# Performance work log

Hardware: AMD Instinct MI355X
Metric: run time of the kernel (lower is better)

## Reference

```python
import jax, jax.numpy as jnp
import numpy as np

N = 100_000
E = 1_600_000
D = 128
LN_EPS = 1e-5


def _gcn_layer(x, src, dst, W, b, gamma, beta):
    # GCNConv (PyG defaults): linear transform, add self-loops, symmetric norm,
    # scatter-add aggregation, then bias. Followed by LayerNorm + ReLU.
    n = x.shape[0]
    h = x @ W  # [N, out]
    loop = jnp.arange(n, dtype=src.dtype)
    src_f = jnp.concatenate([src, loop])  # [E+N]
    dst_f = jnp.concatenate([dst, loop])
    deg = jax.ops.segment_sum(jnp.ones(src_f.shape[0], dtype=h.dtype), dst_f, num_segments=n)
    dinv = jnp.where(deg > 0, jax.lax.rsqrt(deg), 0.0)
    norm = dinv[src_f] * dinv[dst_f]  # [E+N]
    msg = h[src_f] * norm[:, None]  # [E+N, out] -- dominant HBM traffic
    out = jax.ops.segment_sum(msg, dst_f, num_segments=n) + b
    # LayerNorm over feature dim
    mu = jnp.mean(out, axis=-1, keepdims=True)
    var = jnp.mean(jnp.square(out - mu), axis=-1, keepdims=True)
    ln = (out - mu) * jax.lax.rsqrt(var + LN_EPS) * gamma + beta
    # ReLU; dropout is identity in eval mode
    return jax.nn.relu(ln)


def setup_inputs() -> dict:
    key = jax.random.key(0)
    ks = jax.random.split(key, 10)
    x = jax.random.normal(ks[0], (N, D), dtype=jnp.float32)
    edge_index = jax.random.randint(ks[1], (2, E), 0, N, dtype=jnp.int32)
    s = 1.0 / np.sqrt(D)
    W1 = jax.random.normal(ks[2], (D, D), dtype=jnp.float32) * s
    b1 = jnp.zeros((D,), dtype=jnp.float32)
    g1 = jnp.ones((D,), dtype=jnp.float32)
    be1 = jnp.zeros((D,), dtype=jnp.float32)
    W2 = jax.random.normal(ks[3], (D, D), dtype=jnp.float32) * s
    b2 = jnp.zeros((D,), dtype=jnp.float32)
    g2 = jnp.ones((D,), dtype=jnp.float32)
    be2 = jnp.zeros((D,), dtype=jnp.float32)
    return {"x": x, "edge_index": edge_index, "W1": W1, "b1": b1, "g1": g1,
            "be1": be1, "W2": W2, "b2": b2, "g2": g2, "be2": be2}


def reference(x, edge_index, W1, b1, g1, be1, W2, b2, g2, be2):
    src, dst = edge_index[0], edge_index[1]  # PyG flow: source_to_target
    h = _gcn_layer(x, src, dst, W1, b1, g1, be1)
    h = _gcn_layer(h, src, dst, W2, b2, g2, be2)
    return h
```

## Files before the change

### kernel.cpp

```cpp
#include <hip/hip_runtime.h>

#define D 128
#define NBSHIFT 10
#define NB (1 << NBSHIFT)
#define EPB 2048

typedef __attribute__((ext_vector_type(8))) short bf16x8;
typedef __attribute__((ext_vector_type(4))) float floatx4;

__device__ __forceinline__ float bflo(unsigned int u){ return __uint_as_float(u << 16); }
__device__ __forceinline__ float bfhi(unsigned int u){ return __uint_as_float(u & 0xffff0000u); }
__device__ __forceinline__ unsigned int f2bfbits(float f){
    unsigned int x = __float_as_uint(f);
    return (x + 0x7fffu + ((x >> 16) & 1u)) >> 16;
}

__global__ __launch_bounds__(256) void k_bcount(const int* __restrict__ dst, int* __restrict__ bcnt, int E){
    __shared__ int hist[128];
    int t = threadIdx.x;
    int base = blockIdx.x * EPB;
    if (t < 128) hist[t] = 0;
    __syncthreads();
#pragma unroll
    for (int j = 0; j < 8; ++j){
        int e = base + j * 256 + t;
        if (e < E) atomicAdd(&hist[dst[e] >> NBSHIFT], 1);
    }
    __syncthreads();
    if (t < 128 && hist[t] > 0) atomicAdd(&bcnt[t], hist[t]);
}

__global__ void k_bscan(const int* __restrict__ bcnt, int* __restrict__ bbase, int* __restrict__ bcur,
                        int* __restrict__ rowStartN, int NBK){
    if (threadIdx.x == 0){
        int run = 0;
        for (int b = 0; b < NBK; ++b){ bbase[b] = run; bcur[b] = run; run += bcnt[b]; }
        bbase[NBK] = run;
        *rowStartN = run;
    }
}

__global__ __launch_bounds__(256) void k_bucket(const int* __restrict__ src, const int* __restrict__ dst,
                                                int* __restrict__ bcur, unsigned int* __restrict__ edge1,
                                                int NBK, int E){
    __shared__ int hist[128], lstart[128], lcur[128], gbase[128];
    __shared__ unsigned int stage[EPB];
    int t = threadIdx.x;
    int base = blockIdx.x * EPB;
    int tot = min(EPB, E - base);
    if (t < 128) hist[t] = 0;
    __syncthreads();

    unsigned int ent[8]; int bk[8]; int cnt = 0;
#pragma unroll
    for (int j = 0; j < 8; ++j){
        int e = base + j * 256 + t;
        if (e < base + tot){
            unsigned s = (unsigned)src[e], d = (unsigned)dst[e];
            ent[cnt] = s | ((d & (NB - 1)) << 20);
            bk[cnt] = (int)(d >> NBSHIFT);
            atomicAdd(&hist[bk[cnt]], 1);
            ++cnt;
        }
    }
    __syncthreads();
    if (t < 128) lstart[t] = hist[t];
    __syncthreads();
    for (int off = 1; off < 128; off <<= 1){
        int v = 0;
        if (t < 128 && t >= off) v = lstart[t - off];
        __syncthreads();
        if (t < 128) lstart[t] += v;
        __syncthreads();
    }
    if (t < 128){
        int ex = lstart[t] - hist[t];
        lstart[t] = ex;
        lcur[t] = ex;
        if (t < NBK && hist[t] > 0) gbase[t] = atomicAdd(&bcur[t], hist[t]);
    }
    __syncthreads();
    for (int j = 0; j < cnt; ++j){
        int pos = atomicAdd(&lcur[bk[j]], 1);
        stage[pos] = ent[j];
    }
    __syncthreads();
    for (int i = t; i < tot; i += 256){
        unsigned int e1 = stage[i];
        int b = (int)((e1 >> 20) & (NB - 1));
        int lo = 0, hi = 127;
        while (lo < hi){
            int midb = (lo + hi + 1) >> 1;
            if (lstart[midb] <= i) lo = midb; else hi = midb - 1;
        }
        b = lo;
        edge1[gbase[b] + (i - lstart[b])] = e1;
    }
}

__global__ __launch_bounds__(1024) void k_csr2(const unsigned int* __restrict__ edge1,
                                               const int* __restrict__ bbase,
                                               int* __restrict__ rowStart, float* __restrict__ dinv,
                                               int* __restrict__ csr, int N){
    __shared__ int hist[NB];
    __shared__ int sc[NB];
    int b = blockIdx.x, t = threadIdx.x;
    int nbase = b << NBSHIFT;
    int nn = min(N - nbase, NB);
    int ebeg = bbase[b], eend = bbase[b + 1];

    if (t < NB) hist[t] = 0;
    __syncthreads();
    for (int i = ebeg + t; i < eend; i += 1024)
        atomicAdd(&hist[edge1[i] >> 20], 1);
    __syncthreads();
    if (t < NB) sc[t] = hist[t];
    __syncthreads();
    for (int off = 1; off < NB; off <<= 1){
        int v = (t >= off && t < NB) ? sc[t - off] : 0;
        __syncthreads();
        if (t < NB) sc[t] += v;
        __syncthreads();
    }
    if (t < NB){
        int cur = ebeg + sc[t] - hist[t];
        sc[t] = cur;
        if (t < nn){
            rowStart[nbase + t] = cur;
            dinv[nbase + t] = rsqrtf((float)hist[t] + 1.0f);
        }
    }
    __syncthreads();
    for (int i = ebeg + t; i < eend; i += 1024){
        unsigned int p = edge1[i];
        int pos = atomicAdd(&sc[p >> 20], 1);
        csr[pos] = (int)(p & 0xFFFFFu);
    }
}

__global__ __launch_bounds__(256) void k_wtrans(const float* __restrict__ W1,
                                                const float* __restrict__ W2,
                                                unsigned short* __restrict__ Wt1,
                                                unsigned short* __restrict__ Wt2){
    int i = blockIdx.x * 256 + threadIdx.x;
    const float* Ws; unsigned short* Wd; int j = i;
    if (i < 16384){ Ws = W1; Wd = Wt1; } else { Ws = W2; Wd = Wt2; j -= 16384; }
    int k = j >> 7, n = j & 127;
    Wd[n * 128 + k] = (unsigned short)f2bfbits(Ws[k * 128 + n]);
}

template<bool A_BF16>
__global__ __launch_bounds__(256) void k_gemm(const void* __restrict__ Av,
                                              const unsigned short* __restrict__ Wt,
                                              unsigned short* __restrict__ Hout, int Nrows){
    int wave = threadIdx.x >> 6, lane = threadIdx.x & 63;
    int m = lane & 15, quad = lane >> 4;
    int row0 = blockIdx.x * 64 + wave * 16;
    int arow = row0 + m;
    int arowc = arow < Nrows ? arow : Nrows - 1;

    bf16x8 a[4];
    if (A_BF16){
        const unsigned short* Ap = (const unsigned short*)Av + (size_t)arowc * D + quad * 8;
#pragma unroll
        for (int kt = 0; kt < 4; ++kt) a[kt] = *(const bf16x8*)(Ap + kt * 32);
    } else {
        const float* Ap = (const float*)Av + (size_t)arowc * D + quad * 8;
#pragma unroll
        for (int kt = 0; kt < 4; ++kt){
            float4 v0 = *(const float4*)(Ap + kt * 32);
            float4 v1 = *(const float4*)(Ap + kt * 32 + 4);
            bf16x8 af;
            af[0] = (short)f2bfbits(v0.x); af[1] = (short)f2bfbits(v0.y);
            af[2] = (short)f2bfbits(v0.z); af[3] = (short)f2bfbits(v0.w);
            af[4] = (short)f2bfbits(v1.x); af[5] = (short)f2bfbits(v1.y);
            af[6] = (short)f2bfbits(v1.z); af[7] = (short)f2bfbits(v1.w);
            a[kt] = af;
        }
    }

    floatx4 acc[8];
#pragma unroll
    for (int nt = 0; nt < 8; ++nt) acc[nt] = (floatx4){0.f, 0.f, 0.f, 0.f};

    const unsigned short* Bp = Wt + m * D + quad * 8;
#pragma unroll
    for (int kt = 0; kt < 4; ++kt){
        bf16x8 bk[8];
#pragma unroll
        for (int nt = 0; nt < 8; ++nt) bk[nt] = *(const bf16x8*)(Bp + nt * 16 * D + kt * 32);
#pragma unroll
        for (int nt = 0; nt < 8; ++nt)
            acc[nt] = __builtin_amdgcn_mfma_f32_16x16x32_bf16(a[kt], bk[nt], acc[nt], 0, 0, 0);
    }
#pragma unroll
    for (int nt = 0; nt < 8; ++nt){
#pragma unroll
        for (int r = 0; r < 4; ++r){
            int rr = row0 + quad * 4 + r;
            if (rr < Nrows) Hout[(size_t)rr * D + nt * 16 + m] = (unsigned short)f2bfbits(acc[nt][r]);
        }
    }
}

template<bool OUT_BF16>
__global__ __launch_bounds__(256) void k_agg(const unsigned short* __restrict__ h,
                                             const int* __restrict__ rowStart,
                                             const int* __restrict__ csr,
                                             const float* __restrict__ dinv,
                                             const float* __restrict__ bias,
                                             const float* __restrict__ gamma,
                                             const float* __restrict__ beta,
                                             void* __restrict__ outv, int N){
    int node = blockIdx.x * 4 + (threadIdx.x >> 6);
    if (node >= N) return;
    int lane = threadIdx.x & 63;
    int half = lane >> 5, li = lane & 31;
    const uint2* hv = (const uint2*)h;

    float dv = dinv[node];
    float4 acc = {0.f, 0.f, 0.f, 0.f};
    if (half == 0){
        uint2 hs = hv[(size_t)node * 32 + li];
        float w0 = dv * dv;
        acc.x = bflo(hs.x) * w0; acc.y = bfhi(hs.x) * w0;
        acc.z = bflo(hs.y) * w0; acc.w = bfhi(hs.y) * w0;
    }

    int start = rowStart[node], end = rowStart[node + 1];
    int mid = start + ((end - start + 1) >> 1);
    int i    = half ? mid : start;
    int iend = half ? end : mid;

    for (; i + 4 <= iend; i += 4){
        int s0 = csr[i], s1 = csr[i + 1], s2 = csr[i + 2], s3 = csr[i + 3];
        uint2 h0 = hv[(size_t)s0 * 32 + li];
        uint2 h1 = hv[(size_t)s1 * 32 + li];
        uint2 h2 = hv[(size_t)s2 * 32 + li];
        uint2 h3 = hv[(size_t)s3 * 32 + li];
        float w0 = dinv[s0] * dv, w1 = dinv[s1] * dv, w2 = dinv[s2] * dv, w3 = dinv[s3] * dv;
        acc.x = fmaf(bflo(h0.x), w0, acc.x); acc.y = fmaf(bfhi(h0.x), w0, acc.y);
        acc.z = fmaf(bflo(h0.y), w0, acc.z); acc.w = fmaf(bfhi(h0.y), w0, acc.w);
        acc.x = fmaf(bflo(h1.x), w1, acc.x); acc.y = fmaf(bfhi(h1.x), w1, acc.y);
        acc.z = fmaf(bflo(h1.y), w1, acc.z); acc.w = fmaf(bfhi(h1.y), w1, acc.w);
        acc.x = fmaf(bflo(h2.x), w2, acc.x); acc.y = fmaf(bfhi(h2.x), w2, acc.y);
        acc.z = fmaf(bflo(h2.y), w2, acc.z); acc.w = fmaf(bfhi(h2.y), w2, acc.w);
        acc.x = fmaf(bflo(h3.x), w3, acc.x); acc.y = fmaf(bfhi(h3.x), w3, acc.y);
        acc.z = fmaf(bflo(h3.y), w3, acc.z); acc.w = fmaf(bfhi(h3.y), w3, acc.w);
    }
    for (; i < iend; ++i){
        int s = csr[i];
        float ws = dinv[s] * dv;
        uint2 hs = hv[(size_t)s * 32 + li];
        acc.x = fmaf(bflo(hs.x), ws, acc.x); acc.y = fmaf(bfhi(hs.x), ws, acc.y);
        acc.z = fmaf(bflo(hs.y), ws, acc.z); acc.w = fmaf(bfhi(hs.y), ws, acc.w);
    }

    acc.x += __shfl_xor(acc.x, 32, 64);
    acc.y += __shfl_xor(acc.y, 32, 64);
    acc.z += __shfl_xor(acc.z, 32, 64);
    acc.w += __shfl_xor(acc.w, 32, 64);

    float4 bb = ((const float4*)bias)[li];
    acc.x += bb.x; acc.y += bb.y; acc.z += bb.z; acc.w += bb.w;

    float s1 = acc.x + acc.y + acc.z + acc.w;
    float s2 = acc.x * acc.x + acc.y * acc.y + acc.z * acc.z + acc.w * acc.w;
#pragma unroll
    for (int off = 16; off > 0; off >>= 1){
        s1 += __shfl_xor(s1, off, 64);
        s2 += __shfl_xor(s2, off, 64);
    }
    float mu = s1 * (1.0f / 128.0f);
    float var = s2 * (1.0f / 128.0f) - mu * mu;
    float rstd = rsqrtf(var + 1e-5f);

    float4 gg = ((const float4*)gamma)[li];
    float4 be = ((const float4*)beta)[li];
    float ox = fmaxf(fmaf((acc.x - mu) * rstd, gg.x, be.x), 0.0f);
    float oy = fmaxf(fmaf((acc.y - mu) * rstd, gg.y, be.y), 0.0f);
    float oz = fmaxf(fmaf((acc.z - mu) * rstd, gg.z, be.z), 0.0f);
    float ow = fmaxf(fmaf((acc.w - mu) * rstd, gg.w, be.w), 0.0f);
    if (half == 0){
        if (OUT_BF16){
            uint2 o;
            o.x = f2bfbits(ox) | (f2bfbits(oy) << 16);
            o.y = f2bfbits(oz) | (f2bfbits(ow) << 16);
            ((uint2*)outv)[(size_t)node * 32 + li] = o;
        } else {
            floatx4 o = {ox, oy, oz, ow};
            __builtin_nontemporal_store(o, (floatx4*)outv + (size_t)node * 32 + li);
        }
    }
}

extern "C" void kernel_launch(void* const* d_in, const int* in_sizes, int n_in,
                              void* d_out, int out_size, void* d_ws, size_t ws_size,
                              hipStream_t stream){
    const float* x   = (const float*)d_in[0];
    const int*   ei  = (const int*)d_in[1];
    const float* W1  = (const float*)d_in[2];
    const float* b1  = (const float*)d_in[3];
    const float* g1  = (const float*)d_in[4];
    const float* be1 = (const float*)d_in[5];
    const float* W2  = (const float*)d_in[6];
    const float* b2  = (const float*)d_in[7];
    const float* g2  = (const float*)d_in[8];
    const float* be2 = (const float*)d_in[9];
    float* out = (float*)d_out;

    const int N = in_sizes[0] / D;
    const int E = in_sizes[1] / 2;
    const int* src = ei;
    const int* dst = ei + E;

    char* w = (char*)d_ws;
    size_t off = 0;
    auto alloc = [&](size_t bytes) -> char* {
        char* p = w + off;
        off = (off + bytes + 255) & ~(size_t)255;
        return p;
    };
    const int NBK = (N + NB - 1) >> NBSHIFT;
    int*            bcnt     = (int*)alloc((size_t)NBK * 4);
    int*            bbase    = (int*)alloc((size_t)(NBK + 1) * 4);
    int*            bcur     = (int*)alloc((size_t)NBK * 4);
    int*            rowStart = (int*)alloc((size_t)(N + 1) * 4);
    float*          dinv     = (float*)alloc((size_t)N * 4);
    unsigned int*   edge1    = (unsigned int*)alloc((size_t)E * 4);
    int*            csr      = (int*)alloc((size_t)E * 4);
    unsigned short* wt1      = (unsigned short*)alloc(16384 * 2);
    unsigned short* wt2      = (unsigned short*)alloc(16384 * 2);
    unsigned short* h        = (unsigned short*)alloc((size_t)N * D * 2);
    unsigned short* hmid     = (unsigned short*)d_out;

    (void)hipMemsetAsync(bcnt, 0, (size_t)NBK * 4, stream);

    int gB = (E + EPB - 1) / EPB;
    int gG = (N + 63) / 64;
    int gA = (N + 3) / 4;

    k_bcount<<<gB, 256, 0, stream>>>(dst, bcnt, E);
    k_bscan <<<1, 64, 0, stream>>>(bcnt, bbase, bcur, rowStart + N, NBK);
    k_bucket<<<gB, 256, 0, stream>>>(src, dst, bcur, edge1, NBK, E);
    k_csr2  <<<NBK, 1024, 0, stream>>>(edge1, bbase, rowStart, dinv, csr, N);
    k_wtrans<<<128, 256, 0, stream>>>(W1, W2, wt1, wt2);

    k_gemm<false><<<gG, 256, 0, stream>>>(x, wt1, h, N);
    k_agg<true>  <<<gA, 256, 0, stream>>>(h, rowStart, csr, dinv, b1, g1, be1, hmid, N);
    k_gemm<true> <<<gG, 256, 0, stream>>>(hmid, wt2, h, N);
    k_agg<false> <<<gA, 256, 0, stream>>>(h, rowStart, csr, dinv, b2, g2, be2, out, N);
}
```

Measured before the change: 412.5 us.

## Use per-block histograms for deterministic bucketing and coalesce GEMM output via LDS

The edge bucketing pass drops the global atomic counter and the memset. Each block now writes its own histogram, a column-scan kernel computes per-block global offsets, and the bucket kernel writes to those precomputed positions without recounting. The GEMM swaps its operand roles so each lane holds contiguous output columns, stages results in a swizzled LDS tile, and stores full 16-byte rows coalesced instead of scattered 2-byte writes. This adds an extra hist/gloc buffer and a serial column scan over roughly 780 block rows in a single small kernel.

After: 427.0 us. 1.04x slower.

```diff
diff --git a/kernel.cpp b/kernel.cpp
--- a/kernel.cpp
+++ b/kernel.cpp
@@ -15,86 +15,99 @@
     return (x + 0x7fffu + ((x >> 16) & 1u)) >> 16;
 }
 
-__global__ __launch_bounds__(256) void k_bcount(const int* __restrict__ dst, int* __restrict__ bcnt, int E){
-    __shared__ int hist[128];
+__global__ __launch_bounds__(256) void k_bcount(const int* __restrict__ dst,
+                                                int* __restrict__ hist, int E){
+    __shared__ int h[128];
     int t = threadIdx.x;
     int base = blockIdx.x * EPB;
-    if (t < 128) hist[t] = 0;
+    if (t < 128) h[t] = 0;
     __syncthreads();
 #pragma unroll
     for (int j = 0; j < 8; ++j){
         int e = base + j * 256 + t;
-        if (e < E) atomicAdd(&hist[dst[e] >> NBSHIFT], 1);
-    }
-    __syncthreads();
-    if (t < 128 && hist[t] > 0) atomicAdd(&bcnt[t], hist[t]);
-}
-
-__global__ void k_bscan(const int* __restrict__ bcnt, int* __restrict__ bbase, int* __restrict__ bcur,
-                        int* __restrict__ rowStartN, int NBK){
-    if (threadIdx.x == 0){
-        int run = 0;
-        for (int b = 0; b < NBK; ++b){ bbase[b] = run; bcur[b] = run; run += bcnt[b]; }
-        bbase[NBK] = run;
-        *rowStartN = run;
-    }
+        if (e < E) atomicAdd(&h[dst[e] >> NBSHIFT], 1);
+    }
+    __syncthreads();
+    if (t < 128) hist[blockIdx.x * 128 + t] = h[t];
+}
+
+__global__ __launch_bounds__(128) void k_colscan(const int* __restrict__ hist, int nH,
+                                                 int* __restrict__ gloc, int* __restrict__ bbase,
+                                                 int* __restrict__ rowStartN){
+    int b = threadIdx.x;
+    int run = 0;
+    int blk = 0;
+    for (; blk + 4 <= nH; blk += 4){
+        int v0 = hist[(blk + 0) * 128 + b];
+        int v1 = hist[(blk + 1) * 128 + b];
+        int v2 = hist[(blk + 2) * 128 + b];
+        int v3 = hist[(blk + 3) * 128 + b];
+        gloc[(blk + 0) * 128 + b] = run;
+        gloc[(blk + 1) * 128 + b] = run + v0;
+        gloc[(blk + 2) * 128 + b] = run + v0 + v1;
+        gloc[(blk + 3) * 128 + b] = run + v0 + v1 + v2;
+        run += v0 + v1 + v2 + v3;
+    }
+    for (; blk < nH; ++blk){
+        int v = hist[blk * 128 + b];
+        gloc[blk * 128 + b] = run;
+        run += v;
+    }
+    __shared__ int sm[128];
+    sm[b] = run; __syncthreads();
+    for (int off = 1; off < 128; off <<= 1){
+        int x = (b >= off) ? sm[b - off] : 0;
+        __syncthreads();
+        sm[b] += x;
+        __syncthreads();
+    }
+    bbase[b] = (b > 0) ? sm[b - 1] : 0;
+    if (b == 127){ bbase[128] = sm[127]; *rowStartN = sm[127]; }
 }
 
 __global__ __launch_bounds__(256) void k_bucket(const int* __restrict__ src, const int* __restrict__ dst,
-                                                int* __restrict__ bcur, unsigned int* __restrict__ edge1,
-                                                int NBK, int E){
-    __shared__ int hist[128], lstart[128], lcur[128], gbase[128];
+                                                const int* __restrict__ hist, const int* __restrict__ gloc,
+                                                const int* __restrict__ bbase,
+                                                unsigned int* __restrict__ edge1, int E){
+    __shared__ int sc[128], lstart[128], lcur[128], gb[128];
     __shared__ unsigned int stage[EPB];
-    int t = threadIdx.x;
-    int base = blockIdx.x * EPB;
+    int t = threadIdx.x, blk = blockIdx.x;
+    int base = blk * EPB;
     int tot = min(EPB, E - base);
-    if (t < 128) hist[t] = 0;
-    __syncthreads();
-
-    unsigned int ent[8]; int bk[8]; int cnt = 0;
+    int hv = 0;
+    if (t < 128){ hv = hist[blk * 128 + t]; sc[t] = hv; }
+    __syncthreads();
+    for (int off = 1; off < 128; off <<= 1){
+        int v = (t < 128 && t >= off) ? sc[t - off] : 0;
+        __syncthreads();
+        if (t < 128) sc[t] += v;
+        __syncthreads();
+    }
+    if (t < 128){
+        int ex = sc[t] - hv;
+        lstart[t] = ex; lcur[t] = ex;
+        gb[t] = bbase[t] + gloc[blk * 128 + t];
+    }
+    __syncthreads();
 #pragma unroll
     for (int j = 0; j < 8; ++j){
         int e = base + j * 256 + t;
-        if (e < base + tot){
+        if (e < E){
             unsigned s = (unsigned)src[e], d = (unsigned)dst[e];
-            ent[cnt] = s | ((d & (NB - 1)) << 20);
-            bk[cnt] = (int)(d >> NBSHIFT);
-            atomicAdd(&hist[bk[cnt]], 1);
-            ++cnt;
-        }
-    }
-    __syncthreads();
-    if (t < 128) lstart[t] = hist[t];
-    __syncthreads();
-    for (int off = 1; off < 128; off <<= 1){
-        int v = 0;
-        if (t < 128 && t >= off) v = lstart[t - off];
-        __syncthreads();
-        if (t < 128) lstart[t] += v;
-        __syncthreads();
-    }
-    if (t < 128){
-        int ex = lstart[t] - hist[t];
-        lstart[t] = ex;
-        lcur[t] = ex;
-        if (t < NBK && hist[t] > 0) gbase[t] = atomicAdd(&bcur[t], hist[t]);
-    }
-    __syncthreads();
-    for (int j = 0; j < cnt; ++j){
-        int pos = atomicAdd(&lcur[bk[j]], 1);
-        stage[pos] = ent[j];
+            int bk = (int)(d >> NBSHIFT);
+            int pos = atomicAdd(&lcur[bk], 1);
+            stage[pos] = s | ((d & (NB - 1)) << 20);
+        }
     }
     __syncthreads();
     for (int i = t; i < tot; i += 256){
         unsigned int e1 = stage[i];
-        int b = (int)((e1 >> 20) & (NB - 1));
         int lo = 0, hi = 127;
         while (lo < hi){
-            int midb = (lo + hi + 1) >> 1;
-            if (lstart[midb] <= i) lo = midb; else hi = midb - 1;
-        }
-        b = lo;
-        edge1[gbase[b] + (i - lstart[b])] = e1;
+            int m = (lo + hi + 1) >> 1;
+            if (lstart[m] <= i) lo = m; else hi = m - 1;
+        }
+        edge1[gb[lo] + (i - lstart[lo])] = e1;
     }
 }
 
@@ -153,17 +166,18 @@
 __global__ __launch_bounds__(256) void k_gemm(const void* __restrict__ Av,
                                               const unsigned short* __restrict__ Wt,
                                               unsigned short* __restrict__ Hout, int Nrows){
+    __shared__ __align__(16) unsigned short tile[4][2048];
     int wave = threadIdx.x >> 6, lane = threadIdx.x & 63;
-    int m = lane & 15, quad = lane >> 4;
+    int j = lane & 15, quad = lane >> 4;
     int row0 = blockIdx.x * 64 + wave * 16;
-    int arow = row0 + m;
+    int arow = row0 + j;
     int arowc = arow < Nrows ? arow : Nrows - 1;
 
-    bf16x8 a[4];
+    bf16x8 bx[4];
     if (A_BF16){
         const unsigned short* Ap = (const unsigned short*)Av + (size_t)arowc * D + quad * 8;
 #pragma unroll
-        for (int kt = 0; kt < 4; ++kt) a[kt] = *(const bf16x8*)(Ap + kt * 32);
+        for (int kt = 0; kt < 4; ++kt) bx[kt] = *(const bf16x8*)(Ap + kt * 32);
     } else {
         const float* Ap = (const float*)Av + (size_t)arowc * D + quad * 8;
 #pragma unroll
@@ -175,7 +189,7 @@
             af[2] = (short)f2bfbits(v0.z); af[3] = (short)f2bfbits(v0.w);
             af[4] = (short)f2bfbits(v1.x); af[5] = (short)f2bfbits(v1.y);
             af[6] = (short)f2bfbits(v1.z); af[7] = (short)f2bfbits(v1.w);
-            a[kt] = af;
+            bx[kt] = af;
         }
     }
 
@@ -183,23 +197,34 @@
 #pragma unroll
     for (int nt = 0; nt < 8; ++nt) acc[nt] = (floatx4){0.f, 0.f, 0.f, 0.f};
 
-    const unsigned short* Bp = Wt + m * D + quad * 8;
+    const unsigned short* Wp = Wt + j * D + quad * 8;
 #pragma unroll
     for (int kt = 0; kt < 4; ++kt){
-        bf16x8 bk[8];
-#pragma unroll
-        for (int nt = 0; nt < 8; ++nt) bk[nt] = *(const bf16x8*)(Bp + nt * 16 * D + kt * 32);
-#pragma unroll
-        for (int nt = 0; nt < 8; ++nt)
-            acc[nt] = __builtin_amdgcn_mfma_f32_16x16x32_bf16(a[kt], bk[nt], acc[nt], 0, 0, 0);
-    }
+#pragma unroll
+        for (int nt = 0; nt < 8; ++nt){
+            bf16x8 aw = *(const bf16x8*)(Wp + nt * 16 * D + kt * 32);
+            acc[nt] = __builtin_amdgcn_mfma_f32_16x16x32_bf16(aw, bx[kt], acc[nt], 0, 0, 0);
+        }
+    }
+
+    unsigned short* tw = tile[wave];
 #pragma unroll
     for (int nt = 0; nt < 8; ++nt){
-#pragma unroll
-        for (int r = 0; r < 4; ++r){
-            int rr = row0 + quad * 4 + r;
-            if (rr < Nrows) Hout[(size_t)rr * D + nt * 16 + m] = (unsigned short)f2bfbits(acc[nt][r]);
-        }
+        unsigned lo = f2bfbits(acc[nt][0]) | (f2bfbits(acc[nt][1]) << 16);
+        unsigned hi = f2bfbits(acc[nt][2]) | (f2bfbits(acc[nt][3]) << 16);
+        int waddr = j * 256 + nt * 32 + quad * 8;
+        waddr ^= (j & 7) * 32;
+        *(uint2*)((char*)tw + waddr) = make_uint2(lo, hi);
+    }
+    int remb = (Nrows - row0) * 256;
+    char* gout = (char*)Hout + (size_t)row0 * 256;
+#pragma unroll
+    for (int it = 0; it < 4; ++it){
+        int off = it * 1024 + lane * 16;
+        int jr = off >> 8;
+        int raddr = off ^ ((jr & 7) * 32);
+        uint4 v = *(const uint4*)((const char*)tw + raddr);
+        if (off < remb) *(uint4*)(gout + off) = v;
     }
 }
 
@@ -322,9 +347,10 @@
         return p;
     };
     const int NBK = (N + NB - 1) >> NBSHIFT;
-    int*            bcnt     = (int*)alloc((size_t)NBK * 4);
-    int*            bbase    = (int*)alloc((size_t)(NBK + 1) * 4);
-    int*            bcur     = (int*)alloc((size_t)NBK * 4);
+    const int nH  = (E + EPB - 1) / EPB;
+    int*            hist     = (int*)alloc((size_t)nH * 128 * 4);
+    int*            gloc     = (int*)alloc((size_t)nH * 128 * 4);
+    int*            bbase    = (int*)alloc(129 * 4);
     int*            rowStart = (int*)alloc((size_t)(N + 1) * 4);
     float*          dinv     = (float*)alloc((size_t)N * 4);
     unsigned int*   edge1    = (unsigned int*)alloc((size_t)E * 4);
@@ -334,17 +360,14 @@
     unsigned short* h        = (unsigned short*)alloc((size_t)N * D * 2);
     unsigned short* hmid     = (unsigned short*)d_out;
 
-    (void)hipMemsetAsync(bcnt, 0, (size_t)NBK * 4, stream);
-
-    int gB = (E + EPB - 1) / EPB;
     int gG = (N + 63) / 64;
     int gA = (N + 3) / 4;
 
-    k_bcount<<<gB, 256, 0, stream>>>(dst, bcnt, E);
-    k_bscan <<<1, 64, 0, stream>>>(bcnt, bbase, bcur, rowStart + N, NBK);
-    k_bucket<<<gB, 256, 0, stream>>>(src, dst, bcur, edge1, NBK, E);
-    k_csr2  <<<NBK, 1024, 0, stream>>>(edge1, bbase, rowStart, dinv, csr, N);
-    k_wtrans<<<128, 256, 0, stream>>>(W1, W2, wt1, wt2);
+    k_bcount <<<nH, 256, 0, stream>>>(dst, hist, E);
+    k_colscan<<<1, 128, 0, stream>>>(hist, nH, gloc, bbase, rowStart + N);
+    k_bucket <<<nH, 256, 0, stream>>>(src, dst, hist, gloc, bbase, edge1, E);
+    k_csr2   <<<NBK, 1024, 0, stream>>>(edge1, bbase, rowStart, dinv, csr, N);
+    k_wtrans <<<128, 256, 0, stream>>>(W1, W2, wt1, wt2);
 
     k_gemm<false><<<gG, 256, 0, stream>>>(x, wt1, h, N);
     k_agg<true>  <<<gA, 256, 0, stream>>>(h, rowStart, csr, dinv, b1, g1, be1, hmid, N);
```
